# Optimization experiments

Hardware: AMD Instinct MI355X
Metric: run time of the kernel (lower is better)

Reference implementation:

```python
import jax, jax.numpy as jnp
import numpy as np

B, C, H, W = 16, 256, 128, 128  # H must equal W for this module's dilation trick to be consistent
K = 2  # kernel_size (lifting taps)


def setup_inputs() -> dict:
    key = jax.random.key(0)
    ks = jax.random.split(key, 6)
    C4 = C // 4
    return {
        "x": jax.random.normal(ks[0], (B, C, H, W), jnp.float32),
        "conv1x1_w": jax.random.normal(ks[1], (C, C), jnp.float32) / np.sqrt(C).astype(np.float32),
        "lp_v": jax.random.uniform(ks[2], (C4, 1, K, 1), jnp.float32),  # low_pass_filter_v
        "hp_v": jax.random.uniform(ks[3], (C4, 1, K, 1), jnp.float32),  # high_pass_filter_v
        "lp_h": jax.random.uniform(ks[4], (C4, 1, 1, K), jnp.float32),  # low_pass_filter_h
        "hp_h": jax.random.uniform(ks[5], (C4, 1, 1, K), jnp.float32),  # high_pass_filter_h
    }


def _interleave(e, o, axis):
    # interleave e/o along `axis`: out[..., 2i, ...] = e[..., i, ...], out[..., 2i+1, ...] = o[..., i, ...]
    s = jnp.stack([e, o], axis=axis + 1)
    sh = list(e.shape)
    sh[axis] *= 2
    return s.reshape(sh)


def reference(x, conv1x1_w, lp_v, hp_v, lp_h, hp_h):
    # 1x1 conv (no bias)
    x = jnp.einsum('bchw,oc->bohw', x, conv1x1_w)
    b_, c_, h_, w_ = x.shape
    # pad_mode == 'discard': crop to multiple of kernel_size
    x = x[:, :, :h_ - h_ % K, :w_ - w_ % K]
    c4 = c_ // 4
    a = x[:, :c4]
    bq = x[:, c4:2 * c4]
    cq = x[:, 2 * c4:3 * c4]
    dq = x[:, 3 * c4:]
    # per-channel 2-tap combos: w0 * first_half + w1 * second_half
    lv0 = lp_v[:, 0, 0, 0][None, :, None, None]; lv1 = lp_v[:, 0, 1, 0][None, :, None, None]
    hv0 = hp_v[:, 0, 0, 0][None, :, None, None]; hv1 = hp_v[:, 0, 1, 0][None, :, None, None]
    lh0 = lp_h[:, 0, 0, 0][None, :, None, None]; lh1 = lp_h[:, 0, 0, 1][None, :, None, None]
    hh0 = hp_h[:, 0, 0, 0][None, :, None, None]; hh1 = hp_h[:, 0, 0, 1][None, :, None, None]
    # vertical lifting + row interleave -> [B, C/4, 2H, W]
    x_l = _interleave(lv0 * a + lv1 * bq, hv0 * a + hv1 * bq, 2)
    x_h = _interleave(lv0 * cq + lv1 * dq, hv0 * cq + hv1 * dq, 2)
    # horizontal lifting (valid because H == W) + column interleave -> [B, C/4, 2H, 2W]
    x_e = lh0 * x_l + lh1 * x_h
    x_o = hh0 * x_l + hh1 * x_h
    return _interleave(x_e, x_o, 3)
```

## Files before the change

### kernel.cpp

```cpp
#include <hip/hip_runtime.h>

#define HW 16384

typedef __attribute__((ext_vector_type(8))) __bf16 bf16x8;
typedef __attribute__((ext_vector_type(4))) float floatx4;
typedef __attribute__((ext_vector_type(8))) unsigned short ushort8_t;

typedef const __attribute__((address_space(1))) unsigned int gu32;
typedef __attribute__((address_space(3))) unsigned int lu32;

__device__ __forceinline__ unsigned short f2bf(float f) {
    unsigned int u = __builtin_bit_cast(unsigned int, f);
    unsigned int r = (u + 0x7FFFu + ((u >> 16) & 1u)) >> 16;
    return (unsigned short)r;
}

__device__ __forceinline__ void gload_lds16(const unsigned short* g, unsigned short* l) {
    __builtin_amdgcn_global_load_lds((gu32*)g, (lu32*)l, 16, 0, 0);
}

__global__ void wconv_kernel(const float* __restrict__ w, unsigned short* __restrict__ wb) {
    int i = blockIdx.x * 256 + threadIdx.x;
    int row = i >> 8, c = i & 255;
    int kt = c >> 6, kl = c & 63;
    int idx = (row * 64 + kl) ^ ((row & 7) << 3);
    wb[kt * 16384 + idx] = f2bf(w[i]);
}

__global__ __launch_bounds__(512, 4) void fused_gemm_lift(
        const float* __restrict__ x,
        const unsigned short* __restrict__ wb,
        const float* __restrict__ lp_v,
        const float* __restrict__ hp_v,
        const float* __restrict__ lp_h,
        const float* __restrict__ hp_h,
        float* __restrict__ out) {
    __shared__ alignas(16) unsigned short wbuf_s[2][16384];

    const int tid  = threadIdx.x;
    const int wv   = tid >> 6;
    const int lane = tid & 63;
    const int nt   = wv >> 1;
    const int mh   = wv & 1;
    const int tile = blockIdx.x & 255;
    const int bb   = blockIdx.x >> 8;
    const int p0   = tile * 64;

    const int lrow = lane & 15;
    const int kh   = lane >> 4;
    const int fswz = (lrow & 7) << 3;

    const float* xb = x + (size_t)bb * 256 * HW;
    const float* xp = xb + p0 + nt * 16 + lrow;

    floatx4 acc[2][4];
    #pragma unroll
    for (int s = 0; s < 2; ++s)
        #pragma unroll
        for (int g = 0; g < 4; ++g) {
            floatx4 z = {0.f, 0.f, 0.f, 0.f};
            acc[s][g] = z;
        }

    float xf[2][16];

    #pragma unroll
    for (int pass = 0; pass < 4; ++pass) {
        int ch = pass * 512 + wv * 64;
        gload_lds16(wb + (size_t)(ch + lane) * 8, &wbuf_s[0][ch * 8]);
    }
    #pragma unroll
    for (int jj = 0; jj < 16; ++jj) {
        int ch = (jj >> 3) * 32 + kh * 8 + (jj & 7);
        xf[0][jj] = xp[(size_t)ch * HW];
    }
    __syncthreads();

    #pragma unroll
    for (int kt = 0; kt < 4; ++kt) {
        const int cw = kt & 1;

        if (kt < 3) {
            #pragma unroll
            for (int pass = 0; pass < 4; ++pass) {
                int ch = pass * 512 + wv * 64;
                gload_lds16(wb + (size_t)(kt + 1) * 16384 + (size_t)(ch + lane) * 8,
                            &wbuf_s[cw ^ 1][ch * 8]);
            }
            #pragma unroll
            for (int jj = 0; jj < 16; ++jj) {
                int ch = (kt + 1) * 64 + (jj >> 3) * 32 + kh * 8 + (jj & 7);
                xf[cw ^ 1][jj] = xp[(size_t)ch * HW];
            }
        }

        #pragma unroll
        for (int kc = 0; kc < 2; ++kc) {
            ushort8_t u;
            #pragma unroll
            for (int j = 0; j < 8; ++j) u[j] = f2bf(xf[cw][kc * 8 + j]);
            const bf16x8 bfv = __builtin_bit_cast(bf16x8, u);
            #pragma unroll
            for (int s = 0; s < 2; ++s) {
                bf16x8 af[4];
                #pragma unroll
                for (int g = 0; g < 4; ++g) {
                    int row = g * 64 + (mh * 2 + s) * 16 + lrow;
                    af[g] = *reinterpret_cast<const bf16x8*>(
                        &wbuf_s[cw][(row * 64 + kc * 32 + kh * 8) ^ fswz]);
                }
                #pragma unroll
                for (int g = 0; g < 4; ++g)
                    acc[s][g] = __builtin_amdgcn_mfma_f32_16x16x32_bf16(af[g], bfv, acc[s][g], 0, 0, 0);
            }
        }

        if (kt < 3) __syncthreads();
    }

    const int px = p0 + nt * 16 + lrow;
    const int h  = px >> 7;
    const int w  = px & 127;
    #pragma unroll
    for (int s = 0; s < 2; ++s)
        #pragma unroll
        for (int ri = 0; ri < 4; ++ri) {
            const int q = (mh * 2 + s) * 16 + kh * 4 + ri;
            const float lv0 = lp_v[2 * q], lv1 = lp_v[2 * q + 1];
            const float hv0 = hp_v[2 * q], hv1 = hp_v[2 * q + 1];
            const float lh0 = lp_h[2 * q], lh1 = lp_h[2 * q + 1];
            const float hh0 = hp_h[2 * q], hh1 = hp_h[2 * q + 1];
            float* outq = out + (size_t)(bb * 64 + q) * 65536;
            const float a  = acc[s][0][ri];
            const float b2 = acc[s][1][ri];
            const float c2 = acc[s][2][ri];
            const float d2 = acc[s][3][ri];
            const float xl0 = lv0 * a + lv1 * b2;
            const float xl1 = hv0 * a + hv1 * b2;
            const float xh0 = lv0 * c2 + lv1 * d2;
            const float xh1 = hv0 * c2 + hv1 * d2;
            float2 r0 = make_float2(lh0 * xl0 + lh1 * xh0, hh0 * xl0 + hh1 * xh0);
            float2 r1 = make_float2(lh0 * xl1 + lh1 * xh1, hh0 * xl1 + hh1 * xh1);
            *reinterpret_cast<float2*>(outq + (size_t)(2 * h) * 256 + 2 * w)     = r0;
            *reinterpret_cast<float2*>(outq + (size_t)(2 * h + 1) * 256 + 2 * w) = r1;
        }
}

extern "C" void kernel_launch(void* const* d_in, const int* in_sizes, int n_in,
                              void* d_out, int out_size, void* d_ws, size_t ws_size,
                              hipStream_t stream) {
    const float* x   = (const float*)d_in[0];
    const float* w   = (const float*)d_in[1];
    const float* lpv = (const float*)d_in[2];
    const float* hpv = (const float*)d_in[3];
    const float* lph = (const float*)d_in[4];
    const float* hph = (const float*)d_in[5];
    float* outp = (float*)d_out;
    unsigned short* wbp = (unsigned short*)d_ws;

    wconv_kernel<<<dim3(256), dim3(256), 0, stream>>>(w, wbp);
    fused_gemm_lift<<<dim3(4096), dim3(512), 0, stream>>>(x, wbp, lpv, hpv, lph, hph, outp);
}
```

Baseline: 139.8 us.

## Widen pixel tile to 256, load full weight once, use 32x32 MFMA

Each block now covers 256 pixels instead of 64 and loads the whole bf16 weight matrix (128 KB) into LDS once up front. This removes the per-K-step weight double-buffering and the barriers between K steps. Each wave computes all 256 output channels for 32 pixels using 32x32x16 MFMAs with 8 accumulator tiles, and the lifting epilogue is remapped to the 32x32 output layout. The cost is much larger LDS use and register pressure, which lowers occupancy (launch bounds go from 4 to 2), and a quarter as many blocks.

```diff
diff --git a/kernel.cpp b/kernel.cpp
--- a/kernel.cpp
+++ b/kernel.cpp
@@ -3,7 +3,7 @@
 #define HW 16384
 
 typedef __attribute__((ext_vector_type(8))) __bf16 bf16x8;
-typedef __attribute__((ext_vector_type(4))) float floatx4;
+typedef __attribute__((ext_vector_type(16))) float floatx16;
 typedef __attribute__((ext_vector_type(8))) unsigned short ushort8_t;
 
 typedef const __attribute__((address_space(1))) unsigned int gu32;
@@ -27,7 +27,7 @@
     wb[kt * 16384 + idx] = f2bf(w[i]);
 }
 
-__global__ __launch_bounds__(512, 4) void fused_gemm_lift(
+__global__ __launch_bounds__(512, 2) void fused_gemm_lift(
         const float* __restrict__ x,
         const unsigned short* __restrict__ wb,
         const float* __restrict__ lp_v,
@@ -35,45 +35,35 @@
         const float* __restrict__ lp_h,
         const float* __restrict__ hp_h,
         float* __restrict__ out) {
-    __shared__ alignas(16) unsigned short wbuf_s[2][16384];
+    __shared__ alignas(16) unsigned short wbuf_s[4][16384];
 
     const int tid  = threadIdx.x;
     const int wv   = tid >> 6;
     const int lane = tid & 63;
-    const int nt   = wv >> 1;
-    const int mh   = wv & 1;
-    const int tile = blockIdx.x & 255;
-    const int bb   = blockIdx.x >> 8;
-    const int p0   = tile * 64;
+    const int l31  = lane & 31;
+    const int chunk = lane >> 5;
+    const int tile = blockIdx.x & 63;
+    const int bb   = blockIdx.x >> 6;
+    const int p0   = tile * 256;
 
-    const int lrow = lane & 15;
-    const int kh   = lane >> 4;
-    const int fswz = (lrow & 7) << 3;
+    const float* xp = x + (size_t)bb * 256 * HW + p0 + wv * 32 + l31;
 
-    const float* xb = x + (size_t)bb * 256 * HW;
-    const float* xp = xb + p0 + nt * 16 + lrow;
+    floatx16 acc[8];
+    #pragma unroll
+    for (int mt = 0; mt < 8; ++mt)
+        #pragma unroll
+        for (int e = 0; e < 16; ++e) acc[mt][e] = 0.f;
 
-    floatx4 acc[2][4];
-    #pragma unroll
-    for (int s = 0; s < 2; ++s)
-        #pragma unroll
-        for (int g = 0; g < 4; ++g) {
-            floatx4 z = {0.f, 0.f, 0.f, 0.f};
-            acc[s][g] = z;
-        }
-
-    float xf[2][16];
+    float xf[2][32];
 
     #pragma unroll
-    for (int pass = 0; pass < 4; ++pass) {
-        int ch = pass * 512 + wv * 64;
-        gload_lds16(wb + (size_t)(ch + lane) * 8, &wbuf_s[0][ch * 8]);
+    for (int jj = 0; jj < 32; ++jj) {
+        int c = (jj >> 3) * 16 + chunk * 8 + (jj & 7);
+        xf[0][jj] = xp[(size_t)c * HW];
     }
     #pragma unroll
-    for (int jj = 0; jj < 16; ++jj) {
-        int ch = (jj >> 3) * 32 + kh * 8 + (jj & 7);
-        xf[0][jj] = xp[(size_t)ch * HW];
-    }
+    for (int p = 0; p < 16; ++p)
+        gload_lds16(wb + (size_t)(p * 512 + tid) * 8, &wbuf_s[0][0] + (size_t)(p * 512 + tid) * 8);
     __syncthreads();
 
     #pragma unroll
@@ -82,67 +72,57 @@
 
         if (kt < 3) {
             #pragma unroll
-            for (int pass = 0; pass < 4; ++pass) {
-                int ch = pass * 512 + wv * 64;
-                gload_lds16(wb + (size_t)(kt + 1) * 16384 + (size_t)(ch + lane) * 8,
-                            &wbuf_s[cw ^ 1][ch * 8]);
-            }
-            #pragma unroll
-            for (int jj = 0; jj < 16; ++jj) {
-                int ch = (kt + 1) * 64 + (jj >> 3) * 32 + kh * 8 + (jj & 7);
-                xf[cw ^ 1][jj] = xp[(size_t)ch * HW];
+            for (int jj = 0; jj < 32; ++jj) {
+                int c = (kt + 1) * 64 + (jj >> 3) * 16 + chunk * 8 + (jj & 7);
+                xf[cw ^ 1][jj] = xp[(size_t)c * HW];
             }
         }
 
         #pragma unroll
-        for (int kc = 0; kc < 2; ++kc) {
+        for (int k16 = 0; k16 < 4; ++k16) {
             ushort8_t u;
             #pragma unroll
-            for (int j = 0; j < 8; ++j) u[j] = f2bf(xf[cw][kc * 8 + j]);
-            const bf16x8 bfv = __builtin_bit_cast(bf16x8, u);
+            for (int j = 0; j < 8; ++j) u[j] = f2bf(xf[cw][k16 * 8 + j]);
+            const bf16x8 bq = __builtin_bit_cast(bf16x8, u);
+            const int kl = k16 * 16 + chunk * 8;
             #pragma unroll
-            for (int s = 0; s < 2; ++s) {
-                bf16x8 af[4];
-                #pragma unroll
-                for (int g = 0; g < 4; ++g) {
-                    int row = g * 64 + (mh * 2 + s) * 16 + lrow;
-                    af[g] = *reinterpret_cast<const bf16x8*>(
-                        &wbuf_s[cw][(row * 64 + kc * 32 + kh * 8) ^ fswz]);
-                }
-                #pragma unroll
-                for (int g = 0; g < 4; ++g)
-                    acc[s][g] = __builtin_amdgcn_mfma_f32_16x16x32_bf16(af[g], bfv, acc[s][g], 0, 0, 0);
+            for (int mt = 0; mt < 8; ++mt) {
+                const int row = mt * 32 + l31;
+                bf16x8 af = *reinterpret_cast<const bf16x8*>(
+                    &wbuf_s[kt][(row * 64 + kl) ^ ((row & 7) << 3)]);
+                acc[mt] = __builtin_amdgcn_mfma_f32_32x32x16_bf16(af, bq, acc[mt], 0, 0, 0);
             }
         }
-
-        if (kt < 3) __syncthreads();
     }
 
-    const int px = p0 + nt * 16 + lrow;
+    const int px = p0 + wv * 32 + l31;
     const int h  = px >> 7;
     const int w  = px & 127;
+    float* outbase = out + (size_t)bb * 64 * 65536 + (size_t)(2 * h) * 256 + 2 * w;
+    const int hi = lane >> 5;
     #pragma unroll
-    for (int s = 0; s < 2; ++s)
+    for (int mt2 = 0; mt2 < 2; ++mt2)
         #pragma unroll
-        for (int ri = 0; ri < 4; ++ri) {
-            const int q = (mh * 2 + s) * 16 + kh * 4 + ri;
-            const float lv0 = lp_v[2 * q], lv1 = lp_v[2 * q + 1];
-            const float hv0 = hp_v[2 * q], hv1 = hp_v[2 * q + 1];
-            const float lh0 = lp_h[2 * q], lh1 = lp_h[2 * q + 1];
-            const float hh0 = hp_h[2 * q], hh1 = hp_h[2 * q + 1];
-            float* outq = out + (size_t)(bb * 64 + q) * 65536;
-            const float a  = acc[s][0][ri];
-            const float b2 = acc[s][1][ri];
-            const float c2 = acc[s][2][ri];
-            const float d2 = acc[s][3][ri];
-            const float xl0 = lv0 * a + lv1 * b2;
-            const float xl1 = hv0 * a + hv1 * b2;
-            const float xh0 = lv0 * c2 + lv1 * d2;
-            const float xh1 = hv0 * c2 + hv1 * d2;
-            float2 r0 = make_float2(lh0 * xl0 + lh1 * xh0, hh0 * xl0 + hh1 * xh0);
-            float2 r1 = make_float2(lh0 * xl1 + lh1 * xh1, hh0 * xl1 + hh1 * xh1);
-            *reinterpret_cast<float2*>(outq + (size_t)(2 * h) * 256 + 2 * w)     = r0;
-            *reinterpret_cast<float2*>(outq + (size_t)(2 * h + 1) * 256 + 2 * w) = r1;
+        for (int reg = 0; reg < 16; ++reg) {
+            const int row = (reg & 3) + 8 * (reg >> 2) + 4 * hi;
+            const int q = mt2 * 32 + row;
+            const float2 lv = *reinterpret_cast<const float2*>(lp_v + 2 * q);
+            const float2 hv = *reinterpret_cast<const float2*>(hp_v + 2 * q);
+            const float2 lh = *reinterpret_cast<const float2*>(lp_h + 2 * q);
+            const float2 hh = *reinterpret_cast<const float2*>(hp_h + 2 * q);
+            const float a  = acc[mt2][reg];
+            const float b2 = acc[mt2 + 2][reg];
+            const float c2 = acc[mt2 + 4][reg];
+            const float d2 = acc[mt2 + 6][reg];
+            const float xl0 = lv.x * a + lv.y * b2;
+            const float xl1 = hv.x * a + hv.y * b2;
+            const float xh0 = lv.x * c2 + lv.y * d2;
+            const float xh1 = hv.x * c2 + hv.y * d2;
+            float2 r0 = make_float2(lh.x * xl0 + lh.y * xh0, hh.x * xl0 + hh.y * xh0);
+            float2 r1 = make_float2(lh.x * xl1 + lh.y * xh1, hh.x * xl1 + hh.y * xh1);
+            float* oq = outbase + (size_t)q * 65536;
+            *reinterpret_cast<float2*>(oq)       = r0;
+            *reinterpret_cast<float2*>(oq + 256) = r1;
         }
 }
 
@@ -159,5 +139,5 @@
     unsigned short* wbp = (unsigned short*)d_ws;
 
     wconv_kernel<<<dim3(256), dim3(256), 0, stream>>>(w, wbp);
-    fused_gemm_lift<<<dim3(4096), dim3(512), 0, stream>>>(x, wbp, lpv, hpv, lph, hph, outp);
+    fused_gemm_lift<<<dim3(1024), dim3(512), 0, stream>>>(x, wbp, lpv, hpv, lph, hph, outp);
 }
```

Measured after the change: 136.3 us. 2.5% less time.
